# Kernel tuning notes

Measured on AMD Instinct MI355X. Metric: run time of the kernel, lower is better.

## Reference

```python
import jax, jax.numpy as jnp
import numpy as np


def _glorot(key, shape):
    lim = np.sqrt(6.0 / (shape[-2] + shape[-1])).astype(np.float32)
    return jax.random.uniform(key, shape, jnp.float32, -lim, lim)


def setup_inputs() -> dict:
    key = jax.random.key(0)
    B, F, K, L = 8192, 256, 32768, 4
    H = 2 * F          # CouplingLayer(feat_size, feat_size * 2) hidden width
    half = F // 2      # affine coupling transforms half the features
    ks = jax.random.split(key, 6)
    return {
        "inputs": jax.random.normal(ks[0], (B, F), jnp.float32),
        "W1": _glorot(ks[1], (L, half, H)),
        "b1": jnp.zeros((L, H), jnp.float32),
        "Ws": _glorot(ks[2], (L, H, half)),
        "bs": jnp.zeros((L, half), jnp.float32),
        "Wt": _glorot(ks[3], (L, H, half)),
        "bt": jnp.zeros((L, half), jnp.float32),
        "prior": _glorot(ks[4], (K, F)),  # VQ codebook, GlorotUniform init as in source
    }


def _forward_flow(x, W1, b1, Ws, bs, Wt, bt):
    """Stack of affine coupling layers; returns (y, log|det J|) per sample."""
    L = W1.shape[0]
    jac = jnp.zeros((x.shape[0],), x.dtype)
    for l in range(L):  # small fixed layer count
        xa, xb = jnp.split(x, 2, axis=1)                 # [B, F/2] each
        h = jax.nn.relu(xa @ W1[l] + b1[l])              # [B, 2F]
        s_raw = h @ Ws[l] + bs[l]                        # [B, F/2]
        s = s_raw if l == L - 1 else jnp.tanh(s_raw)     # last layer: tf.identity
        t = h @ Wt[l] + bt[l]
        yb = xb * jnp.exp(s) + t
        jac = jac + jnp.sum(s, axis=1)
        x = jnp.concatenate([yb, xa], axis=1)            # swap halves for mixing
    return x, jac


def reference(inputs, W1, b1, Ws, bs, Wt, bt, prior):
    sg = jax.lax.stop_gradient
    x, jac = _forward_flow(inputs, W1, b1, Ws, bs, Wt, bt)   # [B, F], [B]
    # pairwise squared distance to codebook: [B, K]
    na = jnp.sum(x * x, axis=1, keepdims=True)               # [B, 1]
    nb = jnp.sum(prior * prior, axis=1)[None, :]             # [1, K]
    d = jnp.maximum(na - 2.0 * (x @ prior.T) + nb, 0.0)      # [B, K]
    target_ind = jnp.argmin(d, axis=1)                       # [B]
    target = prior[target_ind]                               # gather, [B, F]
    loss_1 = jnp.mean(jnp.sum((x - sg(target)) ** 2, axis=1) / 2)
    loss_2 = jnp.mean(jnp.sum((sg(x) - target) ** 2, axis=1) / 2)
    loss = loss_1 + 0.25 * loss_2 - jnp.mean(jac)
    return x, loss
```

## Files before the change

### kernel.cpp

```cpp
#include <hip/hip_runtime.h>
#include <hip/hip_fp8.h>
#include <stdint.h>

#define NB     8192
#define NF     256
#define NHALF  128
#define NHID   512
#define NLAY   4
#define NK     32768

#define SX     (1.0f / 16.0f)
#define SP     (256.0f)

typedef __attribute__((ext_vector_type(8))) short bf16x8;
typedef __attribute__((ext_vector_type(4))) float f32x4;
typedef __attribute__((ext_vector_type(2))) long i64x2;

static __device__ __forceinline__ unsigned short f2bf(float f) {
  union { float f; unsigned int u; } v; v.f = f;
  return (unsigned short)((v.u + 0x7FFFu + ((v.u >> 16) & 1u)) >> 16);
}
static __device__ __forceinline__ float bf2f(unsigned short u) {
  union { unsigned int u; float f; } v; v.u = ((unsigned int)u) << 16; return v.f;
}
static __device__ __forceinline__ unsigned char f2fp8(float f) {
  __hip_fp8_e4m3 q(f);
  return (unsigned char)q.__x;
}
static __device__ __forceinline__ float fp82f(unsigned char b) {
  __hip_fp8_e4m3 q; q.__x = b; return (float)q;
}
static __device__ __forceinline__ int kperm(int k) {
  return ((k >> 3) & 3) * 64 + ((k >> 5) << 3) + (k & 7);
}

static __device__ __forceinline__ void load_lds16(const void* g, void* l) {
  __builtin_amdgcn_global_load_lds(
      (const __attribute__((address_space(1))) unsigned int*)g,
      (__attribute__((address_space(3))) unsigned int*)l, 16, 0, 0);
}

static __device__ __forceinline__ unsigned long long packsi(float v, int idx) {
  unsigned int b = __float_as_uint(v);
  b = (b & 0x80000000u) ? ~b : (b | 0x80000000u);
  return ((unsigned long long)b << 32) | (unsigned int)(~(unsigned int)idx);
}

static __device__ __forceinline__ float fast_tanh(float x) {
  const float xc = fminf(fmaxf(x, -15.f), 15.f);
  const float e2 = __expf(2.f * xc);
  return 1.f - 2.f / (e2 + 1.f);
}

static __device__ __forceinline__ int swadr(int kseg, int nrows, int row, int kin) {
  return (kseg * nrows + row) * 64 + (((kin >> 3) ^ (row & 7)) * 8) + (kin & 7);
}

__global__ __launch_bounds__(256, 2)
void flow_all(const float* __restrict__ in,
              const unsigned short* __restrict__ W1T,
              const unsigned short* __restrict__ W2I,
              const float* __restrict__ b1A,
              const float* __restrict__ bsA,
              const float* __restrict__ btA,
              float* __restrict__ xout,
              unsigned char* __restrict__ xf8,
              float* __restrict__ jac)
{
  __shared__ __align__(16) unsigned short Xb[2][16 * 128];
  __shared__ __align__(16) unsigned short Hs[16 * 64];
  __shared__ __align__(16) unsigned short Bs[2][8192];
  __shared__ float jlds[3][16];
  const int tid = threadIdx.x;
  const int lane = tid & 63, wave = tid >> 6;
  const int q = lane >> 4, c = lane & 15;
  const int m0 = blockIdx.x * 16;

  {
    const unsigned short* W1l = W1T;
#pragma unroll
    for (int u = 0; u < 4; u++) {
      const int chb = (u * 4 + wave) * 64;
      const int ch = chb + lane;
      const int kseg = ch >> 9, cs = ch & 511;
      const int row = cs >> 3, cc = (cs & 7) ^ (row & 7);
      load_lds16(W1l + (size_t)row * 128 + kseg * 64 + cc * 8, Bs[0] + chb * 8);
    }
  }

#pragma unroll
  for (int v = 0; v < 4; v++) {
    const int t4 = tid + v * 256;
    const int row = t4 >> 6, f4 = t4 & 63;
    const float4 d = *(const float4*)(in + (size_t)(m0 + row) * NF + f4 * 4);
    unsigned short* dst = Xb[f4 >> 5];
    const int feat = (f4 & 31) * 4;
    const float vals[4] = {d.x, d.y, d.z, d.w};
#pragma unroll
    for (int u = 0; u < 4; u++) {
      const int fe = feat + u;
      dst[swadr(fe >> 6, 16, row, fe & 63)] = f2bf(vals[u]);
    }
  }

  float jr[4] = {0.f, 0.f, 0.f, 0.f};
  bf16x8 af1[4];
  const f32x4 z = {0.f, 0.f, 0.f, 0.f};
  f32x4 acc2[4];

  for (int gs = 0; gs < 96; gs++) {
    __syncthreads();

    if (gs + 1 < 96) {
      const int g2 = gs + 1;
      const int l2 = g2 / 24, s2 = g2 % 24, nc2 = s2 / 3, t2 = s2 % 3;
      unsigned short* dst = Bs[g2 & 1];
      if (t2 == 0) {
        const unsigned short* W1l = W1T + (size_t)l2 * (NHID * NHALF) + (size_t)nc2 * 64 * 128;
#pragma unroll
        for (int u = 0; u < 4; u++) {
          const int chb = (u * 4 + wave) * 64;
          const int ch = chb + lane;
          const int kseg = ch >> 9, cs = ch & 511;
          const int row = cs >> 3, cc = (cs & 7) ^ (row & 7);
          load_lds16(W1l + (size_t)row * 128 + kseg * 64 + cc * 8, dst + chb * 8);
        }
      } else {
        const unsigned short* W2l = W2I + (size_t)l2 * (NF * NHID) + nc2 * 64 + (t2 - 1) * 32;
#pragma unroll
        for (int u = 0; u < 4; u++) {
          const int chb = (u * 4 + wave) * 64;
          const int ch = chb + lane;
          const int row = ch >> 2;
          const int cc = (ch & 3) ^ ((row >> 1) & 3);
          load_lds16(W2l + (size_t)row * NHID + cc * 8, dst + chb * 8);
        }
      }
    }

    const int l = gs / 24, s = gs % 24, nc8 = s / 3, typ = s % 3;
    const unsigned short* B = Bs[gs & 1];
    unsigned short* XA = Xb[l & 1];
    unsigned short* XB = Xb[1 - (l & 1)];

    if (typ == 0) {
      if (s == 0) {
#pragma unroll
        for (int kw = 0; kw < 4; kw++) {
          const int kch = kw * 4 + q;
          af1[kw] = *(const bf16x8*)(XA + ((kch >> 3) * 16 + c) * 64 +
                                     (((kch & 7) ^ (c & 7)) * 8));
        }
#pragma unroll
        for (int j = 0; j < 4; j++) acc2[j] = z;
      }
      f32x4 acc1 = z;
      const int rb = wave * 16 + c;
#pragma unroll
      for (int kw = 0; kw < 4; kw++) {
        const int kseg = kw >> 1, g = (kw & 1) * 4 + q;
        const bf16x8 bf = *(const bf16x8*)(B + (kseg * 64 + rb) * 64 + ((g ^ (rb & 7)) * 8));
        acc1 = __builtin_amdgcn_mfma_f32_16x16x32_bf16(af1[kw], bf, acc1, 0, 0, 0);
      }
      const int hc = wave * 16 + c;
      const float bb = b1A[l * NHID + nc8 * 64 + hc];
#pragma unroll
      for (int r = 0; r < 4; r++) {
        float v = acc1[r] + bb;
        v = v > 0.f ? v : 0.f;
        Hs[swadr(0, 16, 4 * q + r, hc)] = f2bf(v);
      }
    } else {
      const int half = typ - 1;
      const bf16x8 afh = *(const bf16x8*)(Hs + c * 64 + (((half * 4 + q) ^ (c & 7)) * 8));
#pragma unroll
      for (int j = 0; j < 4; j++) {
        const int rb = wave * 64 + 16 * j + c;
        const bf16x8 bf = *(const bf16x8*)(B + rb * 32 + ((q ^ ((rb >> 1) & 3)) * 8));
        acc2[j] = __builtin_amdgcn_mfma_f32_16x16x32_bf16(afh, bf, acc2[j], 0, 0, 0);
      }
    }

    if (s == 23) {
      const int parity = c & 1;
      const int lastl = (l == NLAY - 1);
      const float* bsl = bsA + l * NHALF;
      const float* btl = btA + l * NHALF;
#pragma unroll
      for (int j = 0; j < 4; j++) {
        const int col = wave * 64 + 16 * j + c;
#pragma unroll
        for (int r = 0; r < 4; r++) {
          const float val = acc2[j][r];
          const float oth = __shfl_xor(val, 1);
          if (!parity) {
            const int feat = col >> 1;
            float sv = val + bsl[feat];
            if (!lastl) sv = fast_tanh(sv);
            const float t = oth + btl[feat];
            const int row = 4 * q + r;
            const int xaddr = swadr(feat >> 6, 16, row, feat & 63);
            const float xb = bf2f(XB[xaddr]);
            const float yb = xb * __expf(sv) + t;
            jr[r] += sv;
            XB[xaddr] = f2bf(yb);
            if (l >= 2) {
              const int k = lastl ? feat : (NHALF + feat);
              const size_t grow = (size_t)(m0 + row) * NF;
              xout[grow + k] = yb;
              xf8[(size_t)(m0 + row) * 256 + kperm(k)] = f2fp8(yb * SX);
            }
          }
        }
      }
    }
  }

  float v0[4];
#pragma unroll
  for (int r = 0; r < 4; r++) {
    float v = jr[r];
    v += __shfl_xor(v, 1); v += __shfl_xor(v, 2);
    v += __shfl_xor(v, 4); v += __shfl_xor(v, 8);
    if (c == 0) {
      if (wave) jlds[wave - 1][4 * q + r] = v;
      else v0[r] = v;
    }
  }
  __syncthreads();
  if (wave == 0 && c == 0) {
#pragma unroll
    for (int r = 0; r < 4; r++) {
      const int row = 4 * q + r;
      jac[m0 + row] = v0[r] + jlds[0][row] + jlds[1][row] + jlds[2][row];
    }
  }
}

__global__ __launch_bounds__(256, 2)
void vq_argmax(const unsigned char* __restrict__ X8,
               const unsigned char* __restrict__ P8,
               const float* __restrict__ nbh,
               unsigned long long* __restrict__ gbest)
{
  __shared__ __align__(16) unsigned char Bs[64 * 256];
  const int tid = threadIdx.x;
  const int lane = tid & 63, wave = tid >> 6;
  const int y = blockIdx.x & 15;
  const int m0 = (blockIdx.x >> 4) * 256;
  const int q = lane >> 4, c = lane & 15;
  const int mw = m0 + wave * 64;

  long af[4][8];
#pragma unroll
  for (int i = 0; i < 4; i++) {
    const unsigned char* xr = X8 + (size_t)(mw + 16 * i + c) * 256 + q * 64;
#pragma unroll
    for (int kc2 = 0; kc2 < 4; kc2++) {
      const i64x2 v = *(const i64x2*)(xr + kc2 * 16);
      af[i][2 * kc2] = v.x; af[i][2 * kc2 + 1] = v.y;
    }
  }

  float bestv[16];
  int besti[16];
#pragma unroll
  for (int t = 0; t < 16; t++) { bestv[t] = -1e30f; besti[t] = 0; }

  for (int nt = 0; nt < 32; nt++) {
    const int n0 = y * 2048 + nt * 64;
    if (nt) __syncthreads();
#pragma unroll
    for (int u = 0; u < 4; u++) {
      const int chb = (u * 4 + wave) * 64;
      const int ch = chb + lane;
      const int row = ch >> 4, gslot = ch & 15;
      load_lds16(P8 + (size_t)(n0 + row) * 256 + (gslot ^ (row & 15)) * 16,
                 Bs + chb * 16);
    }
    __syncthreads();

    const f32x4 z = {0.f, 0.f, 0.f, 0.f};
    f32x4 acc[4][4];
#pragma unroll
    for (int i = 0; i < 4; i++)
#pragma unroll
      for (int j = 0; j < 4; j++) acc[i][j] = z;

#pragma unroll
    for (int kc2 = 0; kc2 < 4; kc2++) {
      const int g = q * 4 + kc2;
#pragma unroll
      for (int j = 0; j < 4; j++) {
        const int rb = 16 * j + c;
        const i64x2 b2 = *(const i64x2*)(Bs + rb * 256 + ((g ^ (rb & 15)) * 16));
#pragma unroll
        for (int i = 0; i < 4; i++) {
          acc[i][j] = __builtin_amdgcn_mfma_f32_16x16x32_fp8_fp8(af[i][2 * kc2],     b2.x, acc[i][j], 0, 0, 0);
          acc[i][j] = __builtin_amdgcn_mfma_f32_16x16x32_fp8_fp8(af[i][2 * kc2 + 1], b2.y, acc[i][j], 0, 0, 0);
        }
      }
    }

#pragma unroll
    for (int j = 0; j < 4; j++) {
      const int col = n0 + 16 * j + c;
      const float nb = nbh[col];
#pragma unroll
      for (int i = 0; i < 4; i++)
#pragma unroll
        for (int r = 0; r < 4; r++) {
          const float sc = acc[i][j][r] - nb;
          const int t = i * 4 + r;
          if (sc > bestv[t]) { bestv[t] = sc; besti[t] = col; }
        }
    }
  }

#pragma unroll
  for (int t = 0; t < 16; t++) {
    float lv = bestv[t]; int li = besti[t];
#pragma unroll
    for (int mk = 8; mk >= 1; mk >>= 1) {
      const float ov = __shfl_xor(lv, mk);
      const int oi = __shfl_xor(li, mk);
      if (ov > lv || (ov == lv && oi < li)) { lv = ov; li = oi; }
    }
    if (c == 0) {
      const int row = mw + 16 * (t >> 2) + q * 4 + (t & 3);
      atomicMax(&gbest[row], packsi(lv, li));
    }
  }
}

__global__ void prep_all(const float* __restrict__ W1,
                         const float* __restrict__ Ws,
                         const float* __restrict__ Wt,
                         const float* __restrict__ prior,
                         unsigned short* __restrict__ W1T,
                         unsigned short* __restrict__ W2I,
                         unsigned char* __restrict__ p8,
                         float* __restrict__ nbh,
                         unsigned long long* __restrict__ gbest,
                         float* __restrict__ accum)
{
  __shared__ float ts[64 * 65];
  const int bx = blockIdx.x;
  const int tid = threadIdx.x;
  if (bx < 2048) {
    const int k = bx * 16 + (tid >> 4);
    const int l16 = tid & 15;
    float s = 0.f;
#pragma unroll
    for (int v = 0; v < 4; v++) {
      const int off = (v * 16 + l16) * 4;
      const float4 d = *(const float4*)(prior + (size_t)k * NF + off);
      uchar4 o;
      o.x = f2fp8(d.x * SP); o.y = f2fp8(d.y * SP);
      o.z = f2fp8(d.z * SP); o.w = f2fp8(d.w * SP);
      *(uchar4*)(p8 + (size_t)k * 256 + kperm(off)) = o;
      const float q0 = fp82f(o.x), q1 = fp82f(o.y), q2 = fp82f(o.z), q3 = fp82f(o.w);
      s += q0 * q0 + q1 * q1 + q2 * q2 + q3 * q3;
    }
#pragma unroll
    for (int mk = 8; mk >= 1; mk >>= 1) s += __shfl_xor(s, mk);
    if (l16 == 0) nbh[k] = 0.5f * s * (SX / SP);
  } else if (bx < 2112) {
    const int job = bx - 2048;
    const int l = job >> 4, t = job & 15;
    const int k0 = (t >> 3) * 64, n0 = (t & 7) * 64;
    const float* src = W1 + (size_t)l * NHALF * NHID;
#pragma unroll
    for (int v = 0; v < 16; v++) {
      const int e = tid + v * 256;
      const int kk = e >> 6, nn = e & 63;
      ts[kk * 65 + nn] = src[(size_t)(k0 + kk) * NHID + n0 + nn];
    }
    __syncthreads();
    unsigned short* dst = W1T + (size_t)l * NHID * NHALF;
#pragma unroll
    for (int v = 0; v < 16; v++) {
      const int e = tid + v * 256;
      const int nn = e >> 6, kk = e & 63;
      dst[(size_t)(n0 + nn) * NHALF + k0 + kk] = f2bf(ts[kk * 65 + nn]);
    }
  } else if (bx < 2240) {
    const int job = bx - 2112;
    const int l = job >> 5, rem = job & 31;
    const int b = rem >> 4;
    const int k0 = ((rem >> 1) & 7) * 64;
    const int f0 = (rem & 1) * 64;
    const float* src = (b ? Wt : Ws) + (size_t)l * NHID * NHALF;
#pragma unroll
    for (int v = 0; v < 16; v++) {
      const int e = tid + v * 256;
      const int kk = e >> 6, nn = e & 63;
      ts[kk * 65 + nn] = src[(size_t)(k0 + kk) * NHALF + f0 + nn];
    }
    __syncthreads();
#pragma unroll
    for (int v = 0; v < 16; v++) {
      const int e = tid + v * 256;
      const int nn = e >> 6, kk = e & 63;
      W2I[((size_t)l * NF + 2 * (f0 + nn) + b) * NHID + k0 + kk] = f2bf(ts[kk * 65 + nn]);
    }
  } else {
    const int idx = (bx - 2240) * 256 + tid;
    if (idx < NB) gbest[idx] = 0ull;
    if (idx < 2) accum[idx] = 0.f;
  }
}

__global__ void vq_finalize(const float* __restrict__ X,
                            const float* __restrict__ prior,
                            const unsigned long long* __restrict__ gbest,
                            const float* __restrict__ jac,
                            float* __restrict__ accum)
{
  const int wave = threadIdx.x >> 6, lane = threadIdx.x & 63;
  const int gw = blockIdx.x * 4 + wave;
  float accd = 0.f, accj = 0.f;
  for (int r = 0; r < 8; r++) {
    const int row = gw * 8 + r;
    const unsigned int idx = ~(unsigned int)(gbest[row]);
    const float* x = X + (size_t)row * NF;
    const float* p = prior + (size_t)idx * NF;
#pragma unroll
    for (int u = 0; u < 4; u++) {
      const int d = lane + u * 64;
      const float df = x[d] - p[d];
      accd += df * df;
    }
    if (lane == 0) accj += jac[row];
  }
#pragma unroll
  for (int mk = 32; mk >= 1; mk >>= 1) {
    accd += __shfl_xor(accd, mk);
    accj += __shfl_xor(accj, mk);
  }
  __shared__ float sd[4], sj[4];
  if (lane == 0) { sd[wave] = accd; sj[wave] = accj; }
  __syncthreads();
  if (threadIdx.x == 0) {
    atomicAdd(&accum[0], sd[0] + sd[1] + sd[2] + sd[3]);
    atomicAdd(&accum[1], sj[0] + sj[1] + sj[2] + sj[3]);
  }
}

__global__ void finalize_loss(const float* __restrict__ acc, float* __restrict__ loss) {
  if (threadIdx.x == 0 && blockIdx.x == 0)
    loss[0] = 1.25f * (0.5f * acc[0] / (float)NB) - acc[1] / (float)NB;
}

extern "C" void kernel_launch(void* const* d_in, const int* in_sizes, int n_in,
                              void* d_out, int out_size, void* d_ws, size_t ws_size,
                              hipStream_t stream)
{
  (void)in_sizes; (void)n_in; (void)out_size; (void)ws_size;
  const float* inputs = (const float*)d_in[0];
  const float* W1 = (const float*)d_in[1];
  const float* b1 = (const float*)d_in[2];
  const float* Ws = (const float*)d_in[3];
  const float* bs = (const float*)d_in[4];
  const float* Wt = (const float*)d_in[5];
  const float* bt = (const float*)d_in[6];
  const float* prior = (const float*)d_in[7];

  char* p = (char*)d_ws;
  auto alloc = [&](size_t bytes) { char* r = p; p += (bytes + 255) & ~(size_t)255; return r; };
  unsigned short* W1T  = (unsigned short*)alloc((size_t)NLAY * NHID * NHALF * 2);
  unsigned short* W2I  = (unsigned short*)alloc((size_t)NLAY * NF * NHID * 2);
  unsigned char* P8    = (unsigned char*)alloc((size_t)NK * 256);
  float* NBH           = (float*)alloc((size_t)NK * 4);
  unsigned char* XF8   = (unsigned char*)alloc((size_t)NB * 256);
  float* JAC           = (float*)alloc((size_t)NB * 4);
  unsigned long long* GBEST = (unsigned long long*)alloc((size_t)NB * 8);
  float* ACC           = (float*)alloc(256);

  float* xout = (float*)d_out;
  float* loss = xout + (size_t)NB * NF;

  prep_all<<<dim3(2272), 256, 0, stream>>>(
      W1, Ws, Wt, prior, W1T, W2I, P8, NBH, GBEST, ACC);

  flow_all<<<dim3(NB / 16), 256, 0, stream>>>(
      inputs, W1T, W2I, b1, bs, bt, xout, XF8, JAC);

  vq_argmax<<<dim3(32 * 16), 256, 0, stream>>>(XF8, P8, NBH, GBEST);
  vq_finalize<<<dim3(256), 256, 0, stream>>>(xout, prior, GBEST, JAC, ACC);
  finalize_loss<<<1, 1, 0, stream>>>(ACC, loss);
}
```

Before: 291.8 us.

## Restructure flow kernel into larger weight tiles, split VQ grid, fuse loss finalize

The flow kernel drops the 96-step double-buffered pipeline. Each layer now loads 128-column W1 tiles and full-K W2 slabs into one large shared buffer, with syncs between stages. The VQ argmax grid is doubled to 1024 blocks, each scanning half as many codebook entries, and its occupancy hint is raised to 3. The separate finalize_loss launch is replaced by a last-block ticket inside vq_finalize. This trades prefetch overlap and larger shared memory, which may lower flow occupancy, for fewer sync steps and better parallelism in argmax.

```diff
diff --git a/kernel.cpp b/kernel.cpp
--- a/kernel.cpp
+++ b/kernel.cpp
@@ -68,25 +68,13 @@
               float* __restrict__ jac)
 {
   __shared__ __align__(16) unsigned short Xb[2][16 * 128];
-  __shared__ __align__(16) unsigned short Hs[16 * 64];
-  __shared__ __align__(16) unsigned short Bs[2][8192];
+  __shared__ __align__(16) unsigned short Hs[2 * 16 * 64];
+  __shared__ __align__(16) unsigned short Bs[32768];
   __shared__ float jlds[3][16];
   const int tid = threadIdx.x;
   const int lane = tid & 63, wave = tid >> 6;
   const int q = lane >> 4, c = lane & 15;
   const int m0 = blockIdx.x * 16;
-
-  {
-    const unsigned short* W1l = W1T;
-#pragma unroll
-    for (int u = 0; u < 4; u++) {
-      const int chb = (u * 4 + wave) * 64;
-      const int ch = chb + lane;
-      const int kseg = ch >> 9, cs = ch & 511;
-      const int row = cs >> 3, cc = (cs & 7) ^ (row & 7);
-      load_lds16(W1l + (size_t)row * 128 + kseg * 64 + cc * 8, Bs[0] + chb * 8);
-    }
-  }
 
 #pragma unroll
   for (int v = 0; v < 4; v++) {
@@ -104,112 +92,119 @@
   }
 
   float jr[4] = {0.f, 0.f, 0.f, 0.f};
-  bf16x8 af1[4];
   const f32x4 z = {0.f, 0.f, 0.f, 0.f};
-  f32x4 acc2[4];
-
-  for (int gs = 0; gs < 96; gs++) {
+
+  for (int l = 0; l < NLAY; l++) {
     __syncthreads();
-
-    if (gs + 1 < 96) {
-      const int g2 = gs + 1;
-      const int l2 = g2 / 24, s2 = g2 % 24, nc2 = s2 / 3, t2 = s2 % 3;
-      unsigned short* dst = Bs[g2 & 1];
-      if (t2 == 0) {
-        const unsigned short* W1l = W1T + (size_t)l2 * (NHID * NHALF) + (size_t)nc2 * 64 * 128;
-#pragma unroll
-        for (int u = 0; u < 4; u++) {
-          const int chb = (u * 4 + wave) * 64;
-          const int ch = chb + lane;
-          const int kseg = ch >> 9, cs = ch & 511;
-          const int row = cs >> 3, cc = (cs & 7) ^ (row & 7);
-          load_lds16(W1l + (size_t)row * 128 + kseg * 64 + cc * 8, dst + chb * 8);
-        }
-      } else {
-        const unsigned short* W2l = W2I + (size_t)l2 * (NF * NHID) + nc2 * 64 + (t2 - 1) * 32;
-#pragma unroll
-        for (int u = 0; u < 4; u++) {
-          const int chb = (u * 4 + wave) * 64;
-          const int ch = chb + lane;
-          const int row = ch >> 2;
-          const int cc = (ch & 3) ^ ((row >> 1) & 3);
-          load_lds16(W2l + (size_t)row * NHID + cc * 8, dst + chb * 8);
-        }
-      }
-    }
-
-    const int l = gs / 24, s = gs % 24, nc8 = s / 3, typ = s % 3;
-    const unsigned short* B = Bs[gs & 1];
+    const unsigned short* W1l = W1T + (size_t)l * NHID * NHALF;
+    const unsigned short* W2l = W2I + (size_t)l * NF * NHID;
+    const float* bsl = bsA + l * NHALF;
+    const float* btl = btA + l * NHALF;
     unsigned short* XA = Xb[l & 1];
     unsigned short* XB = Xb[1 - (l & 1)];
 
-    if (typ == 0) {
-      if (s == 0) {
-#pragma unroll
-        for (int kw = 0; kw < 4; kw++) {
-          const int kch = kw * 4 + q;
-          af1[kw] = *(const bf16x8*)(XA + ((kch >> 3) * 16 + c) * 64 +
-                                     (((kch & 7) ^ (c & 7)) * 8));
-        }
-#pragma unroll
-        for (int j = 0; j < 4; j++) acc2[j] = z;
-      }
-      f32x4 acc1 = z;
-      const int rb = wave * 16 + c;
+    bf16x8 af1[4];
+#pragma unroll
+    for (int kw = 0; kw < 4; kw++) {
+      const int kch = kw * 4 + q;
+      af1[kw] = *(const bf16x8*)(XA + ((kch >> 3) * 16 + c) * 64 +
+                                 (((kch & 7) ^ (c & 7)) * 8));
+    }
+
+    f32x4 acc2[4];
+#pragma unroll
+    for (int j = 0; j < 4; j++) acc2[j] = z;
+
+    for (int nc = 0; nc < 4; nc++) {
+#pragma unroll
+      for (int u = 0; u < 8; u++) {
+        const int chb = (wave * 8 + u) * 64;
+        const int ch = chb + lane;
+        const int kseg = ch >> 10, cs = ch & 1023;
+        const int row = cs >> 3, cc = (cs & 7) ^ (row & 7);
+        load_lds16(W1l + (size_t)(nc * 128 + row) * NHALF + kseg * 64 + cc * 8,
+                   Bs + chb * 8);
+      }
+      __syncthreads();
+
+      f32x4 acc1[2];
+#pragma unroll
+      for (int j = 0; j < 2; j++) acc1[j] = z;
 #pragma unroll
       for (int kw = 0; kw < 4; kw++) {
         const int kseg = kw >> 1, g = (kw & 1) * 4 + q;
-        const bf16x8 bf = *(const bf16x8*)(B + (kseg * 64 + rb) * 64 + ((g ^ (rb & 7)) * 8));
-        acc1 = __builtin_amdgcn_mfma_f32_16x16x32_bf16(af1[kw], bf, acc1, 0, 0, 0);
-      }
-      const int hc = wave * 16 + c;
-      const float bb = b1A[l * NHID + nc8 * 64 + hc];
+#pragma unroll
+        for (int j = 0; j < 2; j++) {
+          const int rb = wave * 32 + 16 * j + c;
+          const bf16x8 bf = *(const bf16x8*)(Bs + (kseg * 128 + rb) * 64 + ((g ^ (rb & 7)) * 8));
+          acc1[j] = __builtin_amdgcn_mfma_f32_16x16x32_bf16(af1[kw], bf, acc1[j], 0, 0, 0);
+        }
+      }
+#pragma unroll
+      for (int j = 0; j < 2; j++) {
+        const int hc = wave * 32 + 16 * j + c;
+        const float bb = b1A[l * NHID + nc * 128 + hc];
+#pragma unroll
+        for (int r = 0; r < 4; r++) {
+          float v = acc1[j][r] + bb;
+          v = v > 0.f ? v : 0.f;
+          Hs[swadr(hc >> 6, 16, 4 * q + r, hc & 63)] = f2bf(v);
+        }
+      }
+      __syncthreads();
+
+#pragma unroll
+      for (int u = 0; u < 16; u++) {
+        const int chb = u * 256 + wave * 64;
+        const int ch = chb + lane;
+        const int kseg = ch >> 11, cs = ch & 2047;
+        const int row = cs >> 3, cc = (cs & 7) ^ (row & 7);
+        load_lds16(W2l + (size_t)row * NHID + nc * 128 + kseg * 64 + cc * 8,
+                   Bs + chb * 8);
+      }
+      __syncthreads();
+
+#pragma unroll
+      for (int kc = 0; kc < 4; kc++) {
+        const int kch = kc * 4 + q;
+        const int kseg = kch >> 3, g8 = kch & 7;
+        const bf16x8 afh = *(const bf16x8*)(Hs + ((kch >> 3) * 16 + c) * 64 +
+                                            (((kch & 7) ^ (c & 7)) * 8));
+#pragma unroll
+        for (int j = 0; j < 4; j++) {
+          const int rb = wave * 64 + 16 * j + c;
+          const bf16x8 bf = *(const bf16x8*)(Bs + (kseg * 256 + rb) * 64 + ((g8 ^ (rb & 7)) * 8));
+          acc2[j] = __builtin_amdgcn_mfma_f32_16x16x32_bf16(afh, bf, acc2[j], 0, 0, 0);
+        }
+      }
+      __syncthreads();
+    }
+
+    const int parity = c & 1;
+    const int lastl = (l == NLAY - 1);
+#pragma unroll
+    for (int j = 0; j < 4; j++) {
+      const int col = wave * 64 + 16 * j + c;
 #pragma unroll
       for (int r = 0; r < 4; r++) {
-        float v = acc1[r] + bb;
-        v = v > 0.f ? v : 0.f;
-        Hs[swadr(0, 16, 4 * q + r, hc)] = f2bf(v);
-      }
-    } else {
-      const int half = typ - 1;
-      const bf16x8 afh = *(const bf16x8*)(Hs + c * 64 + (((half * 4 + q) ^ (c & 7)) * 8));
-#pragma unroll
-      for (int j = 0; j < 4; j++) {
-        const int rb = wave * 64 + 16 * j + c;
-        const bf16x8 bf = *(const bf16x8*)(B + rb * 32 + ((q ^ ((rb >> 1) & 3)) * 8));
-        acc2[j] = __builtin_amdgcn_mfma_f32_16x16x32_bf16(afh, bf, acc2[j], 0, 0, 0);
-      }
-    }
-
-    if (s == 23) {
-      const int parity = c & 1;
-      const int lastl = (l == NLAY - 1);
-      const float* bsl = bsA + l * NHALF;
-      const float* btl = btA + l * NHALF;
-#pragma unroll
-      for (int j = 0; j < 4; j++) {
-        const int col = wave * 64 + 16 * j + c;
-#pragma unroll
-        for (int r = 0; r < 4; r++) {
-          const float val = acc2[j][r];
-          const float oth = __shfl_xor(val, 1);
-          if (!parity) {
-            const int feat = col >> 1;
-            float sv = val + bsl[feat];
-            if (!lastl) sv = fast_tanh(sv);
-            const float t = oth + btl[feat];
-            const int row = 4 * q + r;
-            const int xaddr = swadr(feat >> 6, 16, row, feat & 63);
-            const float xb = bf2f(XB[xaddr]);
-            const float yb = xb * __expf(sv) + t;
-            jr[r] += sv;
-            XB[xaddr] = f2bf(yb);
-            if (l >= 2) {
-              const int k = lastl ? feat : (NHALF + feat);
-              const size_t grow = (size_t)(m0 + row) * NF;
-              xout[grow + k] = yb;
-              xf8[(size_t)(m0 + row) * 256 + kperm(k)] = f2fp8(yb * SX);
-            }
+        const float val = acc2[j][r];
+        const float oth = __shfl_xor(val, 1);
+        if (!parity) {
+          const int feat = col >> 1;
+          float sv = val + bsl[feat];
+          if (!lastl) sv = fast_tanh(sv);
+          const float t = oth + btl[feat];
+          const int row = 4 * q + r;
+          const int xaddr = swadr(feat >> 6, 16, row, feat & 63);
+          const float xb = bf2f(XB[xaddr]);
+          const float yb = xb * __expf(sv) + t;
+          jr[r] += sv;
+          XB[xaddr] = f2bf(yb);
+          if (l >= 2) {
+            const int k = lastl ? feat : (NHALF + feat);
+            const size_t grow = (size_t)(m0 + row) * NF;
+            xout[grow + k] = yb;
+            xf8[(size_t)(m0 + row) * 256 + kperm(k)] = f2fp8(yb * SX);
           }
         }
       }
@@ -237,7 +232,7 @@
   }
 }
 
-__global__ __launch_bounds__(256, 2)
+__global__ __launch_bounds__(256, 3)
 void vq_argmax(const unsigned char* __restrict__ X8,
                const unsigned char* __restrict__ P8,
                const float* __restrict__ nbh,
@@ -246,10 +241,11 @@
   __shared__ __align__(16) unsigned char Bs[64 * 256];
   const int tid = threadIdx.x;
   const int lane = tid & 63, wave = tid >> 6;
-  const int y = blockIdx.x & 15;
-  const int m0 = (blockIdx.x >> 4) * 256;
+  const int y = (blockIdx.x & 7) + 8 * (blockIdx.x >> 8);
+  const int m0 = ((blockIdx.x >> 3) & 31) * 256;
   const int q = lane >> 4, c = lane & 15;
   const int mw = m0 + wave * 64;
+  const int nbase = y * 1024;
 
   long af[4][8];
 #pragma unroll
@@ -267,8 +263,8 @@
 #pragma unroll
   for (int t = 0; t < 16; t++) { bestv[t] = -1e30f; besti[t] = 0; }
 
-  for (int nt = 0; nt < 32; nt++) {
-    const int n0 = y * 2048 + nt * 64;
+  for (int nt = 0; nt < 16; nt++) {
+    const int n0 = nbase + nt * 64;
     if (nt) __syncthreads();
 #pragma unroll
     for (int u = 0; u < 4; u++) {
@@ -407,7 +403,7 @@
   } else {
     const int idx = (bx - 2240) * 256 + tid;
     if (idx < NB) gbest[idx] = 0ull;
-    if (idx < 2) accum[idx] = 0.f;
+    if (idx < 4) accum[idx] = 0.f;
   }
 }
 
@@ -415,7 +411,8 @@
                             const float* __restrict__ prior,
                             const unsigned long long* __restrict__ gbest,
                             const float* __restrict__ jac,
-                            float* __restrict__ accum)
+                            float* __restrict__ accum,
+                            float* __restrict__ loss)
 {
   const int wave = threadIdx.x >> 6, lane = threadIdx.x & 63;
   const int gw = blockIdx.x * 4 + wave;
@@ -444,12 +441,15 @@
   if (threadIdx.x == 0) {
     atomicAdd(&accum[0], sd[0] + sd[1] + sd[2] + sd[3]);
     atomicAdd(&accum[1], sj[0] + sj[1] + sj[2] + sj[3]);
-  }
-}
-
-__global__ void finalize_loss(const float* __restrict__ acc, float* __restrict__ loss) {
-  if (threadIdx.x == 0 && blockIdx.x == 0)
-    loss[0] = 1.25f * (0.5f * acc[0] / (float)NB) - acc[1] / (float)NB;
+    __threadfence();
+    const unsigned int tk = atomicAdd((unsigned int*)&accum[2], 1u);
+    if (tk == 255u) {
+      __threadfence();
+      const float d = atomicAdd(&accum[0], 0.f);
+      const float j = atomicAdd(&accum[1], 0.f);
+      loss[0] = 1.25f * (0.5f * d / (float)NB) - j / (float)NB;
+    }
+  }
 }
 
 extern "C" void kernel_launch(void* const* d_in, const int* in_sizes, int n_in,
@@ -486,7 +486,6 @@
   flow_all<<<dim3(NB / 16), 256, 0, stream>>>(
       inputs, W1T, W2I, b1, bs, bt, xout, XF8, JAC);
 
-  vq_argmax<<<dim3(32 * 16), 256, 0, stream>>>(XF8, P8, NBH, GBEST);
-  vq_finalize<<<dim3(256), 256, 0, stream>>>(xout, prior, GBEST, JAC, ACC);
-  finalize_loss<<<1, 1, 0, stream>>>(ACC, loss);
-}
+  vq_argmax<<<dim3(1024), 256, 0, stream>>>(XF8, P8, NBH, GBEST);
+  vq_finalize<<<dim3(256), 256, 0, stream>>>(xout, prior, GBEST, JAC, ACC, loss);
+}
```

After: 509.5 us. 74.6% more time.
